# Optimization experiments

Measured on AMD Instinct MI355X. Metric: run time of the kernel, lower is better.

Reference implementation:

```python
import jax, jax.numpy as jnp
import numpy as np
import math

EPS = 1e-5

def _layernorm(x, g, b):
    m = x.mean(-1, keepdims=True)
    v = ((x - m) ** 2).mean(-1, keepdims=True)
    return (x - m) / jnp.sqrt(v + EPS) * g + b

def _skew(emd):
    # RelativePositionalEmbed pad/cat/view skew trick. emd: (B,H,S,S)
    B, H, S, _ = emd.shape
    x = jnp.concatenate([emd, jnp.zeros_like(emd)], -1)   # (B,H,S,2S)
    x = x.reshape(B, H, -1)                                # (B,H,2*S*S)
    l = 2 * S - 1
    extra = (-x.shape[-1]) % l
    x = jnp.concatenate([x, jnp.zeros((B, H, extra), x.dtype)], -1)
    x = x.reshape(B, H, -1, l)
    return x[..., :S, S - 1:]                              # (B,H,S,S)

def setup_inputs() -> dict:
    key = jax.random.key(0)
    ks = jax.random.split(key, 8)
    S, B, D, H, DFF = 1024, 4, 1024, 16, 4096
    dh = D // H
    sc = 1.0 / math.sqrt(D)
    return {
        'x': jax.random.normal(ks[0], (S, B, D), jnp.float32),
        'wq': jax.random.normal(ks[1], (D, D), jnp.float32) * sc,
        'wk': jax.random.normal(ks[2], (D, D), jnp.float32) * sc,
        'wv': jax.random.normal(ks[3], (D, D), jnp.float32) * sc,
        'rel_w': jax.random.normal(ks[4], (B, H, dh, S), jnp.float32) * (1.0 / math.sqrt(dh)),
        'ln1_g': jnp.ones((D,), jnp.float32),
        'ln1_b': jnp.zeros((D,), jnp.float32),
        'ln2_g': jnp.ones((D,), jnp.float32),
        'ln2_b': jnp.zeros((D,), jnp.float32),
        'w1_w': jax.random.normal(ks[5], (DFF, D), jnp.float32) * sc,
        'w1_b': jnp.zeros((DFF,), jnp.float32),
        'w2_w': jax.random.normal(ks[6], (D, DFF), jnp.float32) * (1.0 / math.sqrt(DFF)),
        'w2_b': jnp.zeros((D,), jnp.float32),
    }

def reference(x, wq, wk, wv, rel_w, ln1_g, ln1_b, ln2_g, ln2_b, w1_w, w1_b, w2_w, w2_b):
    S, B, D = x.shape
    H = rel_w.shape[1]
    dh = D // H

    def proj(w):
        y = x @ w.T                      # (S,B,D)
        # torch .view(B,S,H,dh): raw row-major reinterpretation, not a transpose
        return y.reshape(B, S, H, dh).swapaxes(1, 2)  # (B,H,S,dh)

    q, k, v = proj(wq), proj(wk), proj(wv)
    scores = jnp.einsum('bhsd,bhtd->bhst', q * (1.0 / math.sqrt(dh)), k)  # (B,H,S,S)
    # mask=False path: the on-the-fly linear1/linear2 reprojection of qk is
    # computed then discarded in the original; omitted here (dead code).
    emd = jnp.einsum('bhsd,bhdt->bhst', q, rel_w)
    scores = scores + _skew(emd)
    attn = jax.nn.softmax(scores, axis=0)            # softmax over BATCH dim, as in source
    out = jnp.einsum('bhst,bhtd->bhsd', attn, v)     # (B,H,S,dh)
    attn_out = out.reshape(S, B, D)                  # raw reshape, as in source
    h1 = _layernorm(x + attn_out, ln1_g, ln1_b)      # dropout = identity (eval)
    ffn = jnp.maximum(h1 @ w1_w.T + w1_b, 0.0) @ w2_w.T + w2_b
    return _layernorm(h1 + ffn, ln2_g, ln2_b)
```

## Files before the change

### kernel.cpp

```cpp
#include <hip/hip_runtime.h>


typedef unsigned short u16;
typedef unsigned int u32;
typedef __attribute__((ext_vector_type(4))) float f32x4;
typedef __attribute__((ext_vector_type(8))) short bf16x8;

__device__ __forceinline__ float bf2f(u16 u) { return __uint_as_float(((u32)u) << 16); }
__device__ __forceinline__ u16 f2bf(float f) {
    u32 u = __float_as_uint(f);
    u += 0x7fffu + ((u >> 16) & 1u);
    return (u16)(u >> 16);
}
template<int DT>
__device__ __forceinline__ float load1(const void* P, size_t idx) {
    return (DT == 0) ? bf2f(((const u16*)P)[idx]) : ((const float*)P)[idx];
}

__global__ __launch_bounds__(256) void sentinel_ws(float* out, u32 n)
{
    for (u32 i = blockIdx.x * 256 + threadIdx.x; i < n; i += gridDim.x * 256) out[i] = 31000.0f;
}

__global__ __launch_bounds__(256) void cvt_f32_bf16(const float* __restrict__ s,
                                                    u16* __restrict__ d, u32 n)
{
    u32 i = (blockIdx.x * 256 + threadIdx.x) * 4;
    if (i >= n) return;
    float4 v = *(const float4*)(s + i);
    uint2 pk;
    pk.x = (u32)f2bf(v.x) | ((u32)f2bf(v.y) << 16);
    pk.y = (u32)f2bf(v.z) | ((u32)f2bf(v.w) << 16);
    *(uint2*)(d + i) = pk;
}

__global__ __launch_bounds__(256) void relw_tr(const float* __restrict__ relw,
                                               u16* __restrict__ relwT)
{
    __shared__ __align__(16) float T[64][68];
    const int tid = threadIdx.x;
    const int bh = blockIdx.y;
    const int u0 = blockIdx.x << 6;
    {
        const int d = tid >> 2, uq = (tid & 3) << 4;
        const float* rp = relw + (size_t)bh * 65536 + (size_t)d * 1024 + u0 + uq;
#pragma unroll
        for (int i = 0; i < 4; i++)
            *(float4*)&T[d][uq + i * 4] = *(const float4*)(rp + i * 4);
    }
    __syncthreads();
    {
        const int u = tid >> 2, dq = (tid & 3) << 4;
        u32 pk[8];
#pragma unroll
        for (int p = 0; p < 8; p++) {
            float a = T[dq + p * 2][u], b = T[dq + p * 2 + 1][u];
            pk[p] = (u32)f2bf(a) | ((u32)f2bf(b) << 16);
        }
        u16* op = relwT + ((size_t)(bh * 1024 + u0 + u) << 6) + dq;
        *(uint4*)op = *(uint4*)&pk[0];
        *(uint4*)(op + 8) = *(uint4*)&pk[4];
    }
}

__global__ __launch_bounds__(256) void yv_tr(const u16* __restrict__ Yv,
                                             u16* __restrict__ YvT)
{
    __shared__ __align__(16) u16 T[64][72];
    const int tid = threadIdx.x;
    const int bh = blockIdx.y, b = bh >> 4, h = bh & 15;
    const int t0 = blockIdx.x << 6;
    {
        const int r = tid >> 2, cq = (tid & 3) << 4;
        const u16* p = Yv + ((size_t)(b * 1024 + t0 + r) << 10) + h * 64 + cq;
        *(uint4*)&T[r][cq] = *(const uint4*)p;
        *(uint4*)&T[r][cq + 8] = *(const uint4*)(p + 8);
    }
    __syncthreads();
    {
        const int d = tid >> 2, tq = (tid & 3) << 4;
        u16 vals[16];
#pragma unroll
        for (int p = 0; p < 16; p++) vals[p] = T[tq + p][d];
        u16* op = YvT + (((size_t)bh * 64 + d) << 10) + t0 + tq;
        *(uint4*)op = ((uint4*)vals)[0];
        *(uint4*)(op + 8) = ((uint4*)vals)[1];
    }
}

template<int RELU, int OUT_F32, int HAS_BIAS>
__global__ __launch_bounds__(256) void mfma_gemm(
    const u16* __restrict__ A, const u16* __restrict__ B,
    const float* __restrict__ bias, void* __restrict__ Cout,
    int M, int N, int K)
{
    __shared__ __align__(16) u16 As[4096];
    __shared__ __align__(16) u16 Bs[4096];
    const int tid = threadIdx.x;
    const int wave = tid >> 6, lane = tid & 63;
    const int quad = lane >> 4, l16 = lane & 15;
    const int m0 = blockIdx.y << 7, n0 = blockIdx.x << 7;
    const int wm = (wave >> 1) << 6, wn = (wave & 1) << 6;

    const int r0 = tid >> 2;
    const int csw = ((tid & 3) ^ ((r0 >> 1) & 3)) << 3;
    const u16* Ag0 = A + (size_t)(m0 + r0) * K + csw;
    const u16* Ag1 = A + (size_t)(m0 + r0 + 64) * K + csw;
    const u16* Bg0 = B + (size_t)(n0 + r0) * K + csw;
    const u16* Bg1 = B + (size_t)(n0 + r0 + 64) * K + csw;

    f32x4 acc[4][4];
#pragma unroll
    for (int i = 0; i < 4; i++)
#pragma unroll
        for (int j = 0; j < 4; j++) acc[i][j] = (f32x4){0.f, 0.f, 0.f, 0.f};

    const int pb = ((quad ^ ((l16 >> 1) & 3)) << 3);

    uint4 a0 = *(const uint4*)(Ag0);
    uint4 a1 = *(const uint4*)(Ag1);
    uint4 b0 = *(const uint4*)(Bg0);
    uint4 b1 = *(const uint4*)(Bg1);

    for (int k0 = 0; k0 < K; k0 += 32) {
        __syncthreads();
        *(uint4*)(As + tid * 8)        = a0;
        *(uint4*)(As + 2048 + tid * 8) = a1;
        *(uint4*)(Bs + tid * 8)        = b0;
        *(uint4*)(Bs + 2048 + tid * 8) = b1;
        __syncthreads();

        if (k0 + 32 < K) {
            a0 = *(const uint4*)(Ag0 + k0 + 32);
            a1 = *(const uint4*)(Ag1 + k0 + 32);
            b0 = *(const uint4*)(Bg0 + k0 + 32);
            b1 = *(const uint4*)(Bg1 + k0 + 32);
        }

        bf16x8 af[4], bfr[4];
#pragma unroll
        for (int mi = 0; mi < 4; mi++)
            af[mi] = *(const bf16x8*)(As + ((wm + mi * 16 + l16) << 5) + pb);
#pragma unroll
        for (int ni = 0; ni < 4; ni++)
            bfr[ni] = *(const bf16x8*)(Bs + ((wn + ni * 16 + l16) << 5) + pb);
#pragma unroll
        for (int mi = 0; mi < 4; mi++)
#pragma unroll
            for (int ni = 0; ni < 4; ni++)
                acc[mi][ni] = __builtin_amdgcn_mfma_f32_16x16x32_bf16(
                    af[mi], bfr[ni], acc[mi][ni], 0, 0, 0);
    }

    float bb[4];
#pragma unroll
    for (int ni = 0; ni < 4; ni++)
        bb[ni] = HAS_BIAS ? bias[n0 + wn + ni * 16 + l16] : 0.f;

#pragma unroll
    for (int mi = 0; mi < 4; mi++) {
#pragma unroll
        for (int ni = 0; ni < 4; ni++) {
            const int col = n0 + wn + ni * 16 + l16;
#pragma unroll
            for (int r = 0; r < 4; r++) {
                const int row = m0 + wm + mi * 16 + quad * 4 + r;
                float v = acc[mi][ni][r] + bb[ni];
                if (RELU) v = fmaxf(v, 0.f);
                if (OUT_F32) ((float*)Cout)[(size_t)row * N + col] = v;
                else ((u16*)Cout)[(size_t)row * N + col] = f2bf(v);
            }
        }
    }
}

__global__ __launch_bounds__(256) void qk_strip(
    const u16* __restrict__ Yq, const u16* __restrict__ Yk,
    const u16* __restrict__ relwT, u16* __restrict__ scores)
{
    __shared__ __align__(16) u16 lds[26880];
    u16* Ks  = lds;
    u16* Rw  = lds + 4608;
    u16* Eb  = lds + 13824;
    u16* Ssh = lds + 22272;

    const int tid = threadIdx.x;
    const int wave = tid >> 6, lane = tid & 63;
    const int quad = lane >> 4, l16 = lane & 15;
    const int ws = wave >> 1, wt = wave & 1;

    const int linb = blockIdx.y * 16 + blockIdx.x;
    const int swz = (linb & 7) * 128 + (linb >> 3);
    const int si = swz & 15, bh = swz >> 4;
    const int b = bh >> 4, h = bh & 15;
    const int s0 = si << 6;
    const int qb0 = 15 - si;
    const int tau0 = 2 + wt * 2 - ws * 2;

    bf16x8 qf[2][2];
#pragma unroll
    for (int mi = 0; mi < 2; mi++)
#pragma unroll
        for (int kk = 0; kk < 2; kk++)
            qf[mi][kk] = *(const bf16x8*)(Yq +
                ((size_t)(b * 1024 + s0 + ws * 32 + mi * 16 + l16) << 10) +
                h * 64 + kk * 32 + quad * 8);

    const int r = tid >> 2, cq = (tid & 3) << 4;
    const u16* Kg = Yk + ((size_t)(b * 1024 + r) << 10) + h * 64 + cq;
    const u16* Rg = relwT + ((size_t)bh << 16) + cq;

    uint4 kp0, kp1, rp0, rp1, ri0, ri1;
    kp0 = *(const uint4*)(Kg);
    kp1 = *(const uint4*)(Kg + 8);
    {
        const u16* p = Rg + ((size_t)(960 - s0 + r) << 6);
        ri0 = *(const uint4*)p; ri1 = *(const uint4*)(p + 8);
    }
    {
        const int u = 1024 - s0 + r;
        uint4 z = {0, 0, 0, 0};
        rp0 = z; rp1 = z;
        if (u < 1024) {
            const u16* p = Rg + ((size_t)u << 6);
            rp0 = *(const uint4*)p; rp1 = *(const uint4*)(p + 8);
        }
    }

    for (int i = 0; i < 16; i++) {
        const int t0 = i << 6;
        __syncthreads();
        *(uint4*)(Ks + r * 72 + cq)     = kp0;
        *(uint4*)(Ks + r * 72 + cq + 8) = kp1;
        if (i == 0) {
            u16* hb = Rw + (qb0 & 1) * 4608;
            *(uint4*)(hb + r * 72 + cq)     = ri0;
            *(uint4*)(hb + r * 72 + cq + 8) = ri1;
        }
        if (i <= si) {
            u16* hb = Rw + ((qb0 + i + 1) & 1) * 4608;
            *(uint4*)(hb + r * 72 + cq)     = rp0;
            *(uint4*)(hb + r * 72 + cq + 8) = rp1;
        }
        __syncthreads();

        if (i + 1 < 16) {
            const u16* p = Kg + ((size_t)(i + 1) << 16);
            kp0 = *(const uint4*)p; kp1 = *(const uint4*)(p + 8);
        }
        if (i + 1 <= si) {
            const int u = 1024 - s0 + ((i + 1) << 6) + r;
            uint4 z = {0, 0, 0, 0};
            rp0 = z; rp1 = z;
            if (u < 1024) {
                const u16* p = Rg + ((size_t)u << 6);
                rp0 = *(const uint4*)p; rp1 = *(const uint4*)(p + 8);
            }
        }

        f32x4 aqk[2][2];
#pragma unroll
        for (int mi = 0; mi < 2; mi++)
#pragma unroll
            for (int nj = 0; nj < 2; nj++) aqk[mi][nj] = (f32x4){0.f, 0.f, 0.f, 0.f};
#pragma unroll
        for (int kk = 0; kk < 2; kk++)
#pragma unroll
            for (int nj = 0; nj < 2; nj++) {
                bf16x8 kb = *(const bf16x8*)(Ks + (wt * 32 + nj * 16 + l16) * 72 +
                                             kk * 32 + quad * 8);
#pragma unroll
                for (int mi = 0; mi < 2; mi++)
                    aqk[mi][nj] = __builtin_amdgcn_mfma_f32_16x16x32_bf16(
                        qf[mi][kk], kb, aqk[mi][nj], 0, 0, 0);
            }

        const int eact = (i <= si);
        if (eact) {
            const int qb = qb0 + i;
            f32x4 ae[4][2];
#pragma unroll
            for (int uj = 0; uj < 4; uj++)
#pragma unroll
                for (int mi = 0; mi < 2; mi++) ae[uj][mi] = (f32x4){0.f, 0.f, 0.f, 0.f};
#pragma unroll
            for (int kk = 0; kk < 2; kk++)
#pragma unroll
                for (int uj = 0; uj < 4; uj++) {
                    const int tau = tau0 + uj;
                    const u16* hp = Rw + ((qb + (tau >> 2)) & 1) * 4608;
                    bf16x8 ra = *(const bf16x8*)(hp + ((tau & 3) * 16 + l16) * 72 +
                                                 kk * 32 + quad * 8);
#pragma unroll
                    for (int mi = 0; mi < 2; mi++)
                        ae[uj][mi] = __builtin_amdgcn_mfma_f32_16x16x32_bf16(
                            ra, qf[mi][kk], ae[uj][mi], 0, 0, 0);
                }
#pragma unroll
            for (int uj = 0; uj < 4; uj++)
#pragma unroll
                for (int mi = 0; mi < 2; mi++) {
                    const int scol = ws * 32 + mi * 16 + l16;
                    const int cb = (tau0 + uj) * 16 + quad * 4;
                    uint2 pk;
                    pk.x = (u32)f2bf(ae[uj][mi][0]) | ((u32)f2bf(ae[uj][mi][1]) << 16);
                    pk.y = (u32)f2bf(ae[uj][mi][2]) | ((u32)f2bf(ae[uj][mi][3]) << 16);
                    *(uint2*)(Eb + scol * 132 + cb) = pk;
                }
        }

#pragma unroll
        for (int mi = 0; mi < 2; mi++)
#pragma unroll
            for (int nj = 0; nj < 2; nj++)
#pragma unroll
                for (int rr = 0; rr < 4; rr++) {
                    const int sl = ws * 32 + mi * 16 + quad * 4 + rr;
                    const int tl = wt * 32 + nj * 16 + l16;
                    float e = 0.f;
                    if (eact) e = bf2f(Eb[sl * 131 + 63 + tl]);
                    Ssh[sl * 72 + tl] = f2bf(aqk[mi][nj][rr] * 0.125f + e);
                }

        {
            const int row = ws * 32 + (lane >> 1);
            const int col = wt * 32 + ((lane & 1) << 4);
            uint4 v0 = *(const uint4*)(Ssh + row * 72 + col);
            uint4 v1 = *(const uint4*)(Ssh + row * 72 + col + 8);
            u16* op = scores + (((size_t)bh * 1024 + s0 + row) << 10) + t0 + col;
            *(uint4*)op = v0;
            *(uint4*)(op + 8) = v1;
        }
    }
}

__global__ __launch_bounds__(256) void softmax_b(u16* __restrict__ sc)
{
    const size_t e = ((size_t)blockIdx.x * 256 + threadIdx.x) * 8;
    const size_t bs = (size_t)16 * 1024 * 1024;
    uint4 v[4];
#pragma unroll
    for (int bb = 0; bb < 4; bb++) v[bb] = *(const uint4*)(sc + bb * bs + e);
    float x[4][8];
#pragma unroll
    for (int bb = 0; bb < 4; bb++) {
        const u32* w = (const u32*)&v[bb];
#pragma unroll
        for (int j = 0; j < 4; j++) {
            x[bb][2 * j]     = __uint_as_float(w[j] << 16);
            x[bb][2 * j + 1] = __uint_as_float(w[j] & 0xffff0000u);
        }
    }
#pragma unroll
    for (int sl = 0; sl < 8; sl++) {
        float m = fmaxf(fmaxf(x[0][sl], x[1][sl]), fmaxf(x[2][sl], x[3][sl]));
        float ex[4], s = 0.f;
#pragma unroll
        for (int bb = 0; bb < 4; bb++) { ex[bb] = __expf(x[bb][sl] - m); s += ex[bb]; }
        float inv = 1.f / s;
#pragma unroll
        for (int bb = 0; bb < 4; bb++) x[bb][sl] = ex[bb] * inv;
    }
#pragma unroll
    for (int bb = 0; bb < 4; bb++) {
        u32 w[4];
#pragma unroll
        for (int j = 0; j < 4; j++)
            w[j] = (u32)f2bf(x[bb][2 * j]) | ((u32)f2bf(x[bb][2 * j + 1]) << 16);
        *(uint4*)(sc + bb * bs + e) = *(uint4*)w;
    }
}

__global__ __launch_bounds__(256) void pv_mfma(
    const u16* __restrict__ attn, const u16* __restrict__ YvT,
    float* __restrict__ O)
{
    __shared__ __align__(16) u16 Ps[64 * 72];
    __shared__ __align__(16) u16 Vt[64 * 72];
    const int tid = threadIdx.x;
    const int w = tid >> 6, lane = tid & 63;
    const int quad = lane >> 4, l16 = lane & 15;
    const int bh = blockIdx.y;
    const int s0 = blockIdx.x << 6;

    const int sr0 = tid >> 3, sc0 = (tid & 7) << 3;
    const u16* Pg = attn + ((size_t)(bh * 1024 + s0) << 10);
    const u16* Vg = YvT + ((size_t)bh << 16);

    f32x4 acc[4];
#pragma unroll
    for (int i = 0; i < 4; i++) acc[i] = (f32x4){0.f, 0.f, 0.f, 0.f};

    uint4 p0 = *(const uint4*)(Pg + ((size_t)sr0 << 10) + sc0);
    uint4 p1 = *(const uint4*)(Pg + ((size_t)(sr0 + 32) << 10) + sc0);
    uint4 v0 = *(const uint4*)(Vg + ((size_t)sr0 << 10) + sc0);
    uint4 v1 = *(const uint4*)(Vg + ((size_t)(sr0 + 32) << 10) + sc0);

    for (int t0 = 0; t0 < 1024; t0 += 64) {
        __syncthreads();
        *(uint4*)(Ps + sr0 * 72 + sc0) = p0;
        *(uint4*)(Ps + (sr0 + 32) * 72 + sc0) = p1;
        *(uint4*)(Vt + sr0 * 72 + sc0) = v0;
        *(uint4*)(Vt + (sr0 + 32) * 72 + sc0) = v1;
        __syncthreads();

        if (t0 + 64 < 1024) {
            p0 = *(const uint4*)(Pg + ((size_t)sr0 << 10) + t0 + 64 + sc0);
            p1 = *(const uint4*)(Pg + ((size_t)(sr0 + 32) << 10) + t0 + 64 + sc0);
            v0 = *(const uint4*)(Vg + ((size_t)sr0 << 10) + t0 + 64 + sc0);
            v1 = *(const uint4*)(Vg + ((size_t)(sr0 + 32) << 10) + t0 + 64 + sc0);
        }

#pragma unroll
        for (int kk = 0; kk < 2; kk++) {
            bf16x8 af = *(const bf16x8*)(Ps + (w * 16 + l16) * 72 + kk * 32 + quad * 8);
#pragma unroll
            for (int nj = 0; nj < 4; nj++) {
                bf16x8 bv = *(const bf16x8*)(Vt + (nj * 16 + l16) * 72 + kk * 32 + quad * 8);
                acc[nj] = __builtin_amdgcn_mfma_f32_16x16x32_bf16(af, bv, acc[nj], 0, 0, 0);
            }
        }
    }

#pragma unroll
    for (int nj = 0; nj < 4; nj++)
#pragma unroll
        for (int r = 0; r < 4; r++) {
            const int row = s0 + w * 16 + quad * 4 + r;
            O[(((size_t)bh << 10) + row << 6) + nj * 16 + l16] = acc[nj][r];
        }
}

template<int DTA, int OUT_F32>
__global__ __launch_bounds__(256) void add_ln(
    const void* __restrict__ A, const float* __restrict__ Bf,
    const float* __restrict__ g, const float* __restrict__ beta,
    void* __restrict__ out)
{
    const int row = blockIdx.x;
    const int tid = threadIdx.x;
    const size_t base = (size_t)row * 1024;
    float v[4], s1 = 0.f, s2 = 0.f;
#pragma unroll
    for (int k = 0; k < 4; k++) {
        const int c = k * 256 + tid;
        float t = load1<DTA>(A, base + c) + Bf[base + c];
        v[k] = t; s1 += t; s2 += t * t;
    }
#pragma unroll
    for (int m = 1; m < 64; m <<= 1) {
        s1 += __shfl_xor(s1, m, 64);
        s2 += __shfl_xor(s2, m, 64);
    }
    __shared__ float red[8];
    if ((tid & 63) == 0) { red[(tid >> 6) * 2] = s1; red[(tid >> 6) * 2 + 1] = s2; }
    __syncthreads();
    s1 = red[0] + red[2] + red[4] + red[6];
    s2 = red[1] + red[3] + red[5] + red[7];
    const float mean = s1 * (1.f / 1024.f);
    const float var = s2 * (1.f / 1024.f) - mean * mean;
    const float rstd = rsqrtf(var + 1e-5f);
#pragma unroll
    for (int k = 0; k < 4; k++) {
        const int c = k * 256 + tid;
        float o = (v[k] - mean) * rstd * g[c] + beta[c];
        if (OUT_F32) ((float*)out)[base + c] = o;
        else ((u16*)out)[base + c] = f2bf(o);
    }
}

extern "C" void kernel_launch(void* const* d_in, const int* in_sizes, int n_in,
                              void* d_out, int out_size, void* d_ws, size_t ws_size,
                              hipStream_t stream)
{
    const float* x    = (const float*)d_in[0];
    const float* wq   = (const float*)d_in[1];
    const float* wk   = (const float*)d_in[2];
    const float* wv   = (const float*)d_in[3];
    const float* relw = (const float*)d_in[4];
    const float* g1   = (const float*)d_in[5];
    const float* be1  = (const float*)d_in[6];
    const float* g2   = (const float*)d_in[7];
    const float* be2  = (const float*)d_in[8];
    const float* w1   = (const float*)d_in[9];
    const float* b1   = (const float*)d_in[10];
    const float* w2   = (const float*)d_in[11];
    const float* b2   = (const float*)d_in[12];

    const size_t NEEDED = ((size_t)224 << 20);
    if (ws_size < NEEDED) {
        sentinel_ws<<<dim3(1024), dim3(256), 0, stream>>>((float*)d_out, (u32)out_size);
        return;
    }

    char* ws = (char*)d_ws;
    float* O     = (float*)(ws);
    u16*   relwT = (u16*)(ws);
    u16*   Yq    = (u16*)(ws + ((size_t)16 << 20));
    u16*   Yk    = (u16*)(ws + ((size_t)24 << 20));
    u16*   Yv    = (u16*)(ws + ((size_t)32 << 20));
    u16*   h1    = (u16*)(ws + ((size_t)40 << 20));
    u16*   ffn1  = (u16*)(ws + ((size_t)48 << 20));
    float* ffn2  = (float*)(ws + ((size_t)80 << 20));
    u16*   YvT   = (u16*)(ws + ((size_t)80 << 20));
    u16*   sc    = (u16*)(ws + ((size_t)96 << 20));
    u16*   xb    = (u16*)(ws + ((size_t)96 << 20));
    u16*   wqb   = (u16*)(ws + ((size_t)104 << 20));
    u16*   wkb   = (u16*)(ws + ((size_t)106 << 20));
    u16*   wvb   = (u16*)(ws + ((size_t)108 << 20));
    u16*   w1b   = (u16*)(ws + ((size_t)96 << 20));
    u16*   w2b   = (u16*)(ws + ((size_t)104 << 20));

    dim3 blk(256);
    const u32 M4 = 4u << 20, M1 = 1u << 20;

    cvt_f32_bf16<<<dim3(M4 / 1024), blk, 0, stream>>>(x,  xb,  M4);
    cvt_f32_bf16<<<dim3(M1 / 1024), blk, 0, stream>>>(wq, wqb, M1);
    cvt_f32_bf16<<<dim3(M1 / 1024), blk, 0, stream>>>(wk, wkb, M1);
    cvt_f32_bf16<<<dim3(M1 / 1024), blk, 0, stream>>>(wv, wvb, M1);
    relw_tr<<<dim3(16, 64), blk, 0, stream>>>(relw, relwT);

    mfma_gemm<0,0,0><<<dim3(8, 32), blk, 0, stream>>>(xb, wqb, nullptr, Yq, 4096, 1024, 1024);
    mfma_gemm<0,0,0><<<dim3(8, 32), blk, 0, stream>>>(xb, wkb, nullptr, Yk, 4096, 1024, 1024);
    mfma_gemm<0,0,0><<<dim3(8, 32), blk, 0, stream>>>(xb, wvb, nullptr, Yv, 4096, 1024, 1024);
    yv_tr<<<dim3(16, 64), blk, 0, stream>>>(Yv, YvT);

    qk_strip<<<dim3(16, 64), blk, 0, stream>>>(Yq, Yk, relwT, sc);
    softmax_b<<<dim3(8192), blk, 0, stream>>>(sc);
    pv_mfma<<<dim3(16, 64), blk, 0, stream>>>(sc, YvT, O);

    add_ln<1,0><<<dim3(4096), blk, 0, stream>>>(x, O, g1, be1, h1);

    cvt_f32_bf16<<<dim3(M4 / 1024), blk, 0, stream>>>(w1, w1b, M4);
    cvt_f32_bf16<<<dim3(M4 / 1024), blk, 0, stream>>>(w2, w2b, M4);

    mfma_gemm<1,0,1><<<dim3(32, 32), blk, 0, stream>>>(h1, w1b, b1, ffn1, 4096, 4096, 1024);
    mfma_gemm<0,1,1><<<dim3(8, 32), blk, 0, stream>>>(ffn1, w2b, b2, ffn2, 4096, 1024, 4096);

    add_ln<0,1><<<dim3(4096), blk, 0, stream>>>(h1, ffn2, g2, be2, (float*)d_out);
}
```

Baseline: 471.3 us.

## Fuse batch-dim softmax into PV matmul and use packed bf16 conversion

Removes the standalone softmax kernel. The PV kernel now processes all four batches for one head and query strip in a single block, computing the softmax over the batch dimension on the fly from the raw scores in LDS before feeding MFMA. This avoids a full read-modify-write pass over the 128MB bf16 score tensor. It also replaces manual bf16 rounding with the hardware v_cvt_pk_bf16_f32 instruction and pads the Eb LDS stride, presumably to reduce bank conflicts. In exchange the grid shrinks to 256 blocks with 72KB of LDS each, which lowers occupancy and parallelism, and softmax work is recomputed by each wave.

```diff
diff --git a/kernel.cpp b/kernel.cpp
--- a/kernel.cpp
+++ b/kernel.cpp
@@ -11,6 +11,11 @@
     u32 u = __float_as_uint(f);
     u += 0x7fffu + ((u >> 16) & 1u);
     return (u16)(u >> 16);
+}
+__device__ __forceinline__ u32 cvtpk(float lo, float hi) {
+    u32 r;
+    asm("v_cvt_pk_bf16_f32 %0, %1, %2" : "=v"(r) : "v"(lo), "v"(hi));
+    return r;
 }
 template<int DT>
 __device__ __forceinline__ float load1(const void* P, size_t idx) {
@@ -53,10 +58,8 @@
         const int u = tid >> 2, dq = (tid & 3) << 4;
         u32 pk[8];
 #pragma unroll
-        for (int p = 0; p < 8; p++) {
-            float a = T[dq + p * 2][u], b = T[dq + p * 2 + 1][u];
-            pk[p] = (u32)f2bf(a) | ((u32)f2bf(b) << 16);
-        }
+        for (int p = 0; p < 8; p++)
+            pk[p] = cvtpk(T[dq + p * 2][u], T[dq + p * 2 + 1][u]);
         u16* op = relwT + ((size_t)(bh * 1024 + u0 + u) << 6) + dq;
         *(uint4*)op = *(uint4*)&pk[0];
         *(uint4*)(op + 8) = *(uint4*)&pk[4];
@@ -178,11 +181,11 @@
     const u16* __restrict__ Yq, const u16* __restrict__ Yk,
     const u16* __restrict__ relwT, u16* __restrict__ scores)
 {
-    __shared__ __align__(16) u16 lds[26880];
+    __shared__ __align__(16) u16 lds[27008];
     u16* Ks  = lds;
     u16* Rw  = lds + 4608;
     u16* Eb  = lds + 13824;
-    u16* Ssh = lds + 22272;
+    u16* Ssh = lds + 22400;
 
     const int tid = threadIdx.x;
     const int wave = tid >> 6, lane = tid & 63;
@@ -303,24 +306,33 @@
                     const int scol = ws * 32 + mi * 16 + l16;
                     const int cb = (tau0 + uj) * 16 + quad * 4;
                     uint2 pk;
-                    pk.x = (u32)f2bf(ae[uj][mi][0]) | ((u32)f2bf(ae[uj][mi][1]) << 16);
-                    pk.y = (u32)f2bf(ae[uj][mi][2]) | ((u32)f2bf(ae[uj][mi][3]) << 16);
-                    *(uint2*)(Eb + scol * 132 + cb) = pk;
+                    pk.x = cvtpk(ae[uj][mi][0], ae[uj][mi][1]);
+                    pk.y = cvtpk(ae[uj][mi][2], ae[uj][mi][3]);
+                    *(uint2*)(Eb + scol * 134 + cb) = pk;
                 }
         }
 
 #pragma unroll
         for (int mi = 0; mi < 2; mi++)
 #pragma unroll
-            for (int nj = 0; nj < 2; nj++)
+            for (int nj = 0; nj < 2; nj++) {
+                const int slb = ws * 32 + mi * 16 + quad * 4;
+                const int tl = wt * 32 + nj * 16 + l16;
+                float v[4];
 #pragma unroll
                 for (int rr = 0; rr < 4; rr++) {
-                    const int sl = ws * 32 + mi * 16 + quad * 4 + rr;
-                    const int tl = wt * 32 + nj * 16 + l16;
+                    const int sl = slb + rr;
                     float e = 0.f;
-                    if (eact) e = bf2f(Eb[sl * 131 + 63 + tl]);
-                    Ssh[sl * 72 + tl] = f2bf(aqk[mi][nj][rr] * 0.125f + e);
-                }
+                    if (eact) e = bf2f(Eb[sl * 133 + 63 + tl]);
+                    v[rr] = aqk[mi][nj][rr] * 0.125f + e;
+                }
+                const u32 r01 = cvtpk(v[0], v[1]);
+                const u32 r23 = cvtpk(v[2], v[3]);
+                Ssh[(slb + 0) * 72 + tl] = (u16)r01;
+                Ssh[(slb + 1) * 72 + tl] = (u16)(r01 >> 16);
+                Ssh[(slb + 2) * 72 + tl] = (u16)r23;
+                Ssh[(slb + 3) * 72 + tl] = (u16)(r23 >> 16);
+            }
 
         {
             const int row = ws * 32 + (lane >> 1);
@@ -334,101 +346,121 @@
     }
 }
 
-__global__ __launch_bounds__(256) void softmax_b(u16* __restrict__ sc)
-{
-    const size_t e = ((size_t)blockIdx.x * 256 + threadIdx.x) * 8;
-    const size_t bs = (size_t)16 * 1024 * 1024;
-    uint4 v[4];
-#pragma unroll
-    for (int bb = 0; bb < 4; bb++) v[bb] = *(const uint4*)(sc + bb * bs + e);
-    float x[4][8];
-#pragma unroll
-    for (int bb = 0; bb < 4; bb++) {
-        const u32* w = (const u32*)&v[bb];
-#pragma unroll
-        for (int j = 0; j < 4; j++) {
-            x[bb][2 * j]     = __uint_as_float(w[j] << 16);
-            x[bb][2 * j + 1] = __uint_as_float(w[j] & 0xffff0000u);
-        }
-    }
-#pragma unroll
-    for (int sl = 0; sl < 8; sl++) {
-        float m = fmaxf(fmaxf(x[0][sl], x[1][sl]), fmaxf(x[2][sl], x[3][sl]));
-        float ex[4], s = 0.f;
-#pragma unroll
-        for (int bb = 0; bb < 4; bb++) { ex[bb] = __expf(x[bb][sl] - m); s += ex[bb]; }
-        float inv = 1.f / s;
-#pragma unroll
-        for (int bb = 0; bb < 4; bb++) x[bb][sl] = ex[bb] * inv;
-    }
-#pragma unroll
-    for (int bb = 0; bb < 4; bb++) {
-        u32 w[4];
-#pragma unroll
-        for (int j = 0; j < 4; j++)
-            w[j] = (u32)f2bf(x[bb][2 * j]) | ((u32)f2bf(x[bb][2 * j + 1]) << 16);
-        *(uint4*)(sc + bb * bs + e) = *(uint4*)w;
-    }
-}
-
-__global__ __launch_bounds__(256) void pv_mfma(
-    const u16* __restrict__ attn, const u16* __restrict__ YvT,
+__global__ __launch_bounds__(256) void pv_smx(
+    const u16* __restrict__ scraw, const u16* __restrict__ YvT,
     float* __restrict__ O)
 {
-    __shared__ __align__(16) u16 Ps[64 * 72];
-    __shared__ __align__(16) u16 Vt[64 * 72];
+    __shared__ __align__(16) u16 lds[36864];
+    u16* Ps = lds;
+    u16* Vt = lds + 18432;
+
     const int tid = threadIdx.x;
     const int w = tid >> 6, lane = tid & 63;
     const int quad = lane >> 4, l16 = lane & 15;
-    const int bh = blockIdx.y;
-    const int s0 = blockIdx.x << 6;
+
+    const int bid = blockIdx.x;
+    const int swz = (bid & 7) * 32 + (bid >> 3);
+    const int h = swz >> 4, si = swz & 15;
+    const int s0 = si << 6;
 
     const int sr0 = tid >> 3, sc0 = (tid & 7) << 3;
-    const u16* Pg = attn + ((size_t)(bh * 1024 + s0) << 10);
-    const u16* Vg = YvT + ((size_t)bh << 16);
-
-    f32x4 acc[4];
-#pragma unroll
-    for (int i = 0; i < 4; i++) acc[i] = (f32x4){0.f, 0.f, 0.f, 0.f};
-
-    uint4 p0 = *(const uint4*)(Pg + ((size_t)sr0 << 10) + sc0);
-    uint4 p1 = *(const uint4*)(Pg + ((size_t)(sr0 + 32) << 10) + sc0);
-    uint4 v0 = *(const uint4*)(Vg + ((size_t)sr0 << 10) + sc0);
-    uint4 v1 = *(const uint4*)(Vg + ((size_t)(sr0 + 32) << 10) + sc0);
+    const u16* Pg[4]; const u16* Vg[4];
+#pragma unroll
+    for (int b = 0; b < 4; b++) {
+        const int bh = b * 16 + h;
+        Pg[b] = scraw + ((size_t)(bh * 1024 + s0) << 10);
+        Vg[b] = YvT + ((size_t)bh << 16);
+    }
+
+    f32x4 acc[4][4];
+#pragma unroll
+    for (int b = 0; b < 4; b++)
+#pragma unroll
+        for (int j = 0; j < 4; j++) acc[b][j] = (f32x4){0.f, 0.f, 0.f, 0.f};
+
+    uint4 pp[4][2], vv[4][2];
+#pragma unroll
+    for (int b = 0; b < 4; b++) {
+        pp[b][0] = *(const uint4*)(Pg[b] + ((size_t)sr0 << 10) + sc0);
+        pp[b][1] = *(const uint4*)(Pg[b] + ((size_t)(sr0 + 32) << 10) + sc0);
+        vv[b][0] = *(const uint4*)(Vg[b] + ((size_t)sr0 << 10) + sc0);
+        vv[b][1] = *(const uint4*)(Vg[b] + ((size_t)(sr0 + 32) << 10) + sc0);
+    }
 
     for (int t0 = 0; t0 < 1024; t0 += 64) {
         __syncthreads();
-        *(uint4*)(Ps + sr0 * 72 + sc0) = p0;
-        *(uint4*)(Ps + (sr0 + 32) * 72 + sc0) = p1;
-        *(uint4*)(Vt + sr0 * 72 + sc0) = v0;
-        *(uint4*)(Vt + (sr0 + 32) * 72 + sc0) = v1;
+#pragma unroll
+        for (int b = 0; b < 4; b++) {
+            *(uint4*)(Ps + b * 4608 + sr0 * 72 + sc0)        = pp[b][0];
+            *(uint4*)(Ps + b * 4608 + (sr0 + 32) * 72 + sc0) = pp[b][1];
+            *(uint4*)(Vt + b * 4608 + sr0 * 72 + sc0)        = vv[b][0];
+            *(uint4*)(Vt + b * 4608 + (sr0 + 32) * 72 + sc0) = vv[b][1];
+        }
         __syncthreads();
 
         if (t0 + 64 < 1024) {
-            p0 = *(const uint4*)(Pg + ((size_t)sr0 << 10) + t0 + 64 + sc0);
-            p1 = *(const uint4*)(Pg + ((size_t)(sr0 + 32) << 10) + t0 + 64 + sc0);
-            v0 = *(const uint4*)(Vg + ((size_t)sr0 << 10) + t0 + 64 + sc0);
-            v1 = *(const uint4*)(Vg + ((size_t)(sr0 + 32) << 10) + t0 + 64 + sc0);
+#pragma unroll
+            for (int b = 0; b < 4; b++) {
+                pp[b][0] = *(const uint4*)(Pg[b] + ((size_t)sr0 << 10) + t0 + 64 + sc0);
+                pp[b][1] = *(const uint4*)(Pg[b] + ((size_t)(sr0 + 32) << 10) + t0 + 64 + sc0);
+                vv[b][0] = *(const uint4*)(Vg[b] + ((size_t)sr0 << 10) + t0 + 64 + sc0);
+                vv[b][1] = *(const uint4*)(Vg[b] + ((size_t)(sr0 + 32) << 10) + t0 + 64 + sc0);
+            }
         }
 
 #pragma unroll
         for (int kk = 0; kk < 2; kk++) {
-            bf16x8 af = *(const bf16x8*)(Ps + (w * 16 + l16) * 72 + kk * 32 + quad * 8);
-#pragma unroll
-            for (int nj = 0; nj < 4; nj++) {
-                bf16x8 bv = *(const bf16x8*)(Vt + (nj * 16 + l16) * 72 + kk * 32 + quad * 8);
-                acc[nj] = __builtin_amdgcn_mfma_f32_16x16x32_bf16(af, bv, acc[nj], 0, 0, 0);
-            }
-        }
-    }
-
-#pragma unroll
-    for (int nj = 0; nj < 4; nj++)
-#pragma unroll
-        for (int r = 0; r < 4; r++) {
-            const int row = s0 + w * 16 + quad * 4 + r;
-            O[(((size_t)bh << 10) + row << 6) + nj * 16 + l16] = acc[nj][r];
-        }
+            bf16x8 ar[4];
+#pragma unroll
+            for (int b = 0; b < 4; b++)
+                ar[b] = *(const bf16x8*)(Ps + b * 4608 + (w * 16 + l16) * 72 +
+                                         kk * 32 + quad * 8);
+            bf16x8 a[4];
+#pragma unroll
+            for (int j = 0; j < 4; j++) {
+                float x0[4], x1[4];
+#pragma unroll
+                for (int b = 0; b < 4; b++) {
+                    x0[b] = bf2f((u16)ar[b][2 * j]);
+                    x1[b] = bf2f((u16)ar[b][2 * j + 1]);
+                }
+                const float m0 = fmaxf(fmaxf(x0[0], x0[1]), fmaxf(x0[2], x0[3]));
+                const float m1 = fmaxf(fmaxf(x1[0], x1[1]), fmaxf(x1[2], x1[3]));
+                float s0v = 0.f, s1v = 0.f;
+#pragma unroll
+                for (int b = 0; b < 4; b++) {
+                    x0[b] = __expf(x0[b] - m0); s0v += x0[b];
+                    x1[b] = __expf(x1[b] - m1); s1v += x1[b];
+                }
+                const float r0 = 1.f / s0v, r1 = 1.f / s1v;
+#pragma unroll
+                for (int b = 0; b < 4; b++) {
+                    u32 wd = cvtpk(x0[b] * r0, x1[b] * r1);
+                    ((u32*)&a[b])[j] = wd;
+                }
+            }
+#pragma unroll
+            for (int b = 0; b < 4; b++)
+#pragma unroll
+                for (int nj = 0; nj < 4; nj++) {
+                    bf16x8 bv = *(const bf16x8*)(Vt + b * 4608 + (nj * 16 + l16) * 72 +
+                                                 kk * 32 + quad * 8);
+                    acc[b][nj] = __builtin_amdgcn_mfma_f32_16x16x32_bf16(
+                        a[b], bv, acc[b][nj], 0, 0, 0);
+                }
+        }
+    }
+
+#pragma unroll
+    for (int b = 0; b < 4; b++)
+#pragma unroll
+        for (int nj = 0; nj < 4; nj++)
+#pragma unroll
+            for (int rr = 0; rr < 4; rr++) {
+                const int row = s0 + w * 16 + quad * 4 + rr;
+                O[((((size_t)(b * 16 + h) << 10) + row) << 6) + nj * 16 + l16] =
+                    acc[b][nj][rr];
+            }
 }
 
 template<int DTA, int OUT_F32>
@@ -526,8 +558,7 @@
     yv_tr<<<dim3(16, 64), blk, 0, stream>>>(Yv, YvT);
 
     qk_strip<<<dim3(16, 64), blk, 0, stream>>>(Yq, Yk, relwT, sc);
-    softmax_b<<<dim3(8192), blk, 0, stream>>>(sc);
-    pv_mfma<<<dim3(16, 64), blk, 0, stream>>>(sc, YvT, O);
+    pv_smx<<<dim3(256), blk, 0, stream>>>(sc, YvT, O);
 
     add_ln<1,0><<<dim3(4096), blk, 0, stream>>>(x, O, g1, be1, h1);
 
```

New measurement: 544.0 us. +15.4%, slower.
